# Optimization experiments

Measured on AMD Instinct MI355X. Metric: run time of the kernel, lower is better.

Reference implementation:

```python
import jax, jax.numpy as jnp
import numpy as np

SHIFT = 1  # shift_direction fixed to +1 (original picks +/-1 randomly at init)


def setup_inputs() -> dict:
    key = jax.random.key(0)
    kx, kw = jax.random.split(key)
    x = jax.random.normal(kx, (128, 128, 56, 56), dtype=jnp.float32)  # (N, C, H, W)
    w = jax.random.normal(kw, (32, 3, 128), dtype=jnp.float32)        # (out_ch, ktap, in_ch)
    return {"x": x, "w": w}


def reference(x, w):
    # roll along W (original dim 3), then 1x3 conv along W with SAME padding,
    # then roll the output along H (original dim 2).
    xr = jnp.roll(x, SHIFT, axis=3)
    # einsum 'nkmilo,jki->njmlo' == correlation: y[n,j,h,w] = sum_{k,i} xr[n,i,h,w+k-1] * w[j,k,i]
    kernel = jnp.transpose(w, (0, 2, 1))[:, :, None, :]  # (O=32, I=128, kh=1, kw=3)
    y = jax.lax.conv_general_dilated(
        xr, kernel,
        window_strides=(1, 1),
        padding=((0, 0), (1, 1)),
        dimension_numbers=("NCHW", "OIHW", "NCHW"),
    )  # (128, 32, 56, 56)
    return jnp.roll(y, SHIFT, axis=2)
```

## Files before the change

### kernel.cpp

```cpp
#include <hip/hip_runtime.h>
#include <stddef.h>


#define C_IN   128
#define C_OUT  32
#define HH     56
#define WW     56
#define HW     3136
#define KTOT   384
#define WSTRIDE 392
#define XSTRIDE 136
#define XROWSZ (57 * XSTRIDE)

typedef short bf16x8 __attribute__((ext_vector_type(8)));
typedef float f32x4  __attribute__((ext_vector_type(4)));

static __device__ __forceinline__ unsigned short f2b(float f) {
    unsigned u = __builtin_bit_cast(unsigned, f);
    unsigned r = u + 0x7FFFu + ((u >> 16) & 1u);
    return (unsigned short)(r >> 16);
}

__global__ void pack_w_kernel(const float* __restrict__ w, unsigned short* __restrict__ ws) {
    int idx = blockIdx.x * 256 + threadIdx.x;
    if (idx < C_OUT * WSTRIDE) {
        int j = idx / WSTRIDE;
        int r = idx % WSTRIDE;
        ws[idx] = f2b(r < KTOT ? w[j * KTOT + r] : 0.0f);
    }
}

__global__ __launch_bounds__(256, 2)
void conv_mfma_kernel(const float* __restrict__ x, const unsigned short* __restrict__ ws,
                      float* __restrict__ out) {
    const int bid  = blockIdx.x;
    const int n    = bid / (HH / 4);
    const int h0   = (bid % (HH / 4)) * 4;
    const int tid  = threadIdx.x;
    const int lane = tid & 63;
    const int grp  = tid >> 6;

    __shared__ __align__(16) unsigned short XT[4 * XROWSZ];

    if (tid < 68) {
        int r = tid / 17, off = (tid % 17) * 8;
        *(uint4*)&XT[r * XROWSZ + WW * XSTRIDE + off] = make_uint4(0, 0, 0, 0);
    }

    const float* xb = x + (size_t)n * (C_IN * HW);

    {
        const int q  = lane;
        const int r  = q / 14;
        const int c4 = q % 14;
        const int hs = (h0 + 55 + r) % HH;
        const size_t rowoff = (size_t)hs * WW + c4 * 4;
        unsigned short* dst0 = &XT[r * XROWSZ + (c4 * 4) * XSTRIDE];
#pragma unroll 8
        for (int p = 0; p < 32; ++p) {
            const int ch = p * 4 + grp;
            if (q < WW) {
                const float4 v = *(const float4*)(xb + (size_t)ch * HW + rowoff);
                unsigned short* dst = dst0 + ch;
                dst[0]           = f2b(v.x);
                dst[XSTRIDE]     = f2b(v.y);
                dst[2 * XSTRIDE] = f2b(v.z);
                dst[3 * XSTRIDE] = f2b(v.w);
            }
        }
    }
    __syncthreads();

    const int l15 = lane & 15;
    const int kb  = (lane >> 4) * 8;
    const unsigned short* Xr = &XT[grp * XROWSZ];

    const unsigned short* bp[4][3];
#pragma unroll
    for (int ct = 0; ct < 4; ++ct) {
        const int nn = ct * 16 + l15;
        const int cc0 = (nn >= 1 && nn <= 55) ? (nn + 54) % WW : WW;
        const int cc1 = (nn <= 55) ? (nn + 55) % WW : WW;
        const int cc2 = (nn <= 54) ? nn : WW;
        bp[ct][0] = Xr + cc0 * XSTRIDE + kb;
        bp[ct][1] = Xr + cc1 * XSTRIDE + kb;
        bp[ct][2] = Xr + cc2 * XSTRIDE + kb;
    }

    const unsigned short* wp = ws + l15 * WSTRIDE + kb;

    f32x4 acc[4][2];
#pragma unroll
    for (int ct = 0; ct < 4; ++ct) {
        acc[ct][0] = (f32x4){0.f, 0.f, 0.f, 0.f};
        acc[ct][1] = (f32x4){0.f, 0.f, 0.f, 0.f};
    }

#pragma unroll
    for (int c = 0; c < 12; ++c) {
        const int tap = c >> 2;
        const int ib  = (c & 3) * 32;
        bf16x8 A0 = *(const bf16x8*)(wp + c * 32);
        bf16x8 A1 = *(const bf16x8*)(wp + 16 * WSTRIDE + c * 32);
#pragma unroll
        for (int ct = 0; ct < 4; ++ct) {
            bf16x8 B = *(const bf16x8*)(bp[ct][tap] + ib);
            acc[ct][0] = __builtin_amdgcn_mfma_f32_16x16x32_bf16(A0, B, acc[ct][0], 0, 0, 0);
            acc[ct][1] = __builtin_amdgcn_mfma_f32_16x16x32_bf16(A1, B, acc[ct][1], 0, 0, 0);
        }
    }

    {
        const int h  = h0 + grp;
        const int j0 = (lane >> 4) * 4;
        float* ob = out + (size_t)n * (C_OUT * HW) + (size_t)h * WW;
#pragma unroll
        for (int ct = 0; ct < 4; ++ct) {
            const int nn = ct * 16 + l15;
            if (nn < WW) {
#pragma unroll
                for (int r = 0; r < 4; ++r) {
                    ob[(size_t)(j0 + r) * HW + nn]      = acc[ct][0][r];
                    ob[(size_t)(j0 + r + 16) * HW + nn] = acc[ct][1][r];
                }
            }
        }
    }
}

extern "C" void kernel_launch(void* const* d_in, const int* in_sizes, int n_in,
                              void* d_out, int out_size, void* d_ws, size_t ws_size,
                              hipStream_t stream) {
    const float* x = (const float*)d_in[0];
    const float* w = (const float*)d_in[1];
    float* out = (float*)d_out;
    unsigned short* ws = (unsigned short*)d_ws;

    pack_w_kernel<<<(C_OUT * WSTRIDE + 255) / 256, 256, 0, stream>>>(w, ws);
    conv_mfma_kernel<<<dim3(128 * (HH / 4)), dim3(256), 0, stream>>>(x, ws, out);
}
```

Measured before the change: 304.5 us.

## Double block size to 512 threads, splitting each row's columns across two waves

Raises the conv kernel's block size from 256 to 512 threads (8 waves). The staging loop now has 8 waves each loading 16 channels, and in the compute phase two waves share each output row, each handling half of the column tiles. The aim is more waves in flight to hide global-load latency during staging, with fewer accumulators per thread. In exchange each wave reuses its A-fragment weight loads across fewer MFMAs, and the launch bounds now request 4 blocks of 512 threads per CU, which may be limited by LDS.

```diff
diff --git a/kernel.cpp b/kernel.cpp
--- a/kernel.cpp
+++ b/kernel.cpp
@@ -30,7 +30,7 @@
     }
 }
 
-__global__ __launch_bounds__(256, 2)
+__global__ __launch_bounds__(512, 4)
 void conv_mfma_kernel(const float* __restrict__ x, const unsigned short* __restrict__ ws,
                       float* __restrict__ out) {
     const int bid  = blockIdx.x;
@@ -55,13 +55,13 @@
         const int c4 = q % 14;
         const int hs = (h0 + 55 + r) % HH;
         const size_t rowoff = (size_t)hs * WW + c4 * 4;
-        unsigned short* dst0 = &XT[r * XROWSZ + (c4 * 4) * XSTRIDE];
+        unsigned short* dst0 = &XT[r * XROWSZ + (c4 * 4) * XSTRIDE + grp];
+        const float* src0 = xb + (size_t)grp * HW + rowoff;
 #pragma unroll 8
-        for (int p = 0; p < 32; ++p) {
-            const int ch = p * 4 + grp;
+        for (int p = 0; p < 16; ++p) {
             if (q < WW) {
-                const float4 v = *(const float4*)(xb + (size_t)ch * HW + rowoff);
-                unsigned short* dst = dst0 + ch;
+                const float4 v = *(const float4*)(src0 + (size_t)(p * 8) * HW);
+                unsigned short* dst = dst0 + p * 8;
                 dst[0]           = f2b(v.x);
                 dst[XSTRIDE]     = f2b(v.y);
                 dst[2 * XSTRIDE] = f2b(v.z);
@@ -73,27 +73,29 @@
 
     const int l15 = lane & 15;
     const int kb  = (lane >> 4) * 8;
-    const unsigned short* Xr = &XT[grp * XROWSZ];
+    const int rr  = grp >> 1;
+    const int hf  = grp & 1;
+    const unsigned short* Xr = &XT[rr * XROWSZ];
 
-    const unsigned short* bp[4][3];
+    const unsigned short* bp[2][3];
 #pragma unroll
-    for (int ct = 0; ct < 4; ++ct) {
-        const int nn = ct * 16 + l15;
+    for (int ct2 = 0; ct2 < 2; ++ct2) {
+        const int nn = (hf * 2 + ct2) * 16 + l15;
         const int cc0 = (nn >= 1 && nn <= 55) ? (nn + 54) % WW : WW;
         const int cc1 = (nn <= 55) ? (nn + 55) % WW : WW;
         const int cc2 = (nn <= 54) ? nn : WW;
-        bp[ct][0] = Xr + cc0 * XSTRIDE + kb;
-        bp[ct][1] = Xr + cc1 * XSTRIDE + kb;
-        bp[ct][2] = Xr + cc2 * XSTRIDE + kb;
+        bp[ct2][0] = Xr + cc0 * XSTRIDE + kb;
+        bp[ct2][1] = Xr + cc1 * XSTRIDE + kb;
+        bp[ct2][2] = Xr + cc2 * XSTRIDE + kb;
     }
 
     const unsigned short* wp = ws + l15 * WSTRIDE + kb;
 
-    f32x4 acc[4][2];
+    f32x4 acc[2][2];
 #pragma unroll
-    for (int ct = 0; ct < 4; ++ct) {
-        acc[ct][0] = (f32x4){0.f, 0.f, 0.f, 0.f};
-        acc[ct][1] = (f32x4){0.f, 0.f, 0.f, 0.f};
+    for (int ct2 = 0; ct2 < 2; ++ct2) {
+        acc[ct2][0] = (f32x4){0.f, 0.f, 0.f, 0.f};
+        acc[ct2][1] = (f32x4){0.f, 0.f, 0.f, 0.f};
     }
 
 #pragma unroll
@@ -103,25 +105,25 @@
         bf16x8 A0 = *(const bf16x8*)(wp + c * 32);
         bf16x8 A1 = *(const bf16x8*)(wp + 16 * WSTRIDE + c * 32);
 #pragma unroll
-        for (int ct = 0; ct < 4; ++ct) {
-            bf16x8 B = *(const bf16x8*)(bp[ct][tap] + ib);
-            acc[ct][0] = __builtin_amdgcn_mfma_f32_16x16x32_bf16(A0, B, acc[ct][0], 0, 0, 0);
-            acc[ct][1] = __builtin_amdgcn_mfma_f32_16x16x32_bf16(A1, B, acc[ct][1], 0, 0, 0);
+        for (int ct2 = 0; ct2 < 2; ++ct2) {
+            bf16x8 B = *(const bf16x8*)(bp[ct2][tap] + ib);
+            acc[ct2][0] = __builtin_amdgcn_mfma_f32_16x16x32_bf16(A0, B, acc[ct2][0], 0, 0, 0);
+            acc[ct2][1] = __builtin_amdgcn_mfma_f32_16x16x32_bf16(A1, B, acc[ct2][1], 0, 0, 0);
         }
     }
 
     {
-        const int h  = h0 + grp;
+        const int h  = h0 + rr;
         const int j0 = (lane >> 4) * 4;
         float* ob = out + (size_t)n * (C_OUT * HW) + (size_t)h * WW;
 #pragma unroll
-        for (int ct = 0; ct < 4; ++ct) {
-            const int nn = ct * 16 + l15;
+        for (int ct2 = 0; ct2 < 2; ++ct2) {
+            const int nn = (hf * 2 + ct2) * 16 + l15;
             if (nn < WW) {
 #pragma unroll
                 for (int r = 0; r < 4; ++r) {
-                    ob[(size_t)(j0 + r) * HW + nn]      = acc[ct][0][r];
-                    ob[(size_t)(j0 + r + 16) * HW + nn] = acc[ct][1][r];
+                    ob[(size_t)(j0 + r) * HW + nn]      = acc[ct2][0][r];
+                    ob[(size_t)(j0 + r + 16) * HW + nn] = acc[ct2][1][r];
                 }
             }
         }
@@ -137,5 +139,5 @@
     unsigned short* ws = (unsigned short*)d_ws;
 
     pack_w_kernel<<<(C_OUT * WSTRIDE + 255) / 256, 256, 0, stream>>>(w, ws);
-    conv_mfma_kernel<<<dim3(128 * (HH / 4)), dim3(256), 0, stream>>>(x, ws, out);
+    conv_mfma_kernel<<<dim3(128 * (HH / 4)), dim3(512), 0, stream>>>(x, ws, out);
 }
```

Measured after the change: 307.9 us. No clear change (+1.1%).

## Use single-wave workgroups per row with packed bf16 LDS stores and XCD swizzle

Applied to the files above, without the earlier changes.

Restructures the conv kernel from 4-wave blocks covering four output rows to one-wave blocks handling a single row, which removes the block barrier in favour of an lgkmcnt wait. The staging loop now loads 8 channels per lane and converts pairs with v_cvt_pk_bf16_f32, writing 128-bit LDS stores instead of scalar 16-bit stores. Block indices are remapped so consecutive workgroups spread across the 8 XCDs. The change targets the cost of staging and conversion plus synchronization, at the price of smaller blocks and more workgroups to schedule.

```diff
diff --git a/kernel.cpp b/kernel.cpp
--- a/kernel.cpp
+++ b/kernel.cpp
@@ -21,6 +21,12 @@
     return (unsigned short)(r >> 16);
 }
 
+static __device__ __forceinline__ unsigned pk2(float lo, float hi) {
+    unsigned r;
+    asm("v_cvt_pk_bf16_f32 %0, %1, %2" : "=v"(r) : "v"(lo), "v"(hi));
+    return r;
+}
+
 __global__ void pack_w_kernel(const float* __restrict__ w, unsigned short* __restrict__ ws) {
     int idx = blockIdx.x * 256 + threadIdx.x;
     if (idx < C_OUT * WSTRIDE) {
@@ -30,50 +36,49 @@
     }
 }
 
-__global__ __launch_bounds__(256, 2)
+__global__ __launch_bounds__(64, 4)
 void conv_mfma_kernel(const float* __restrict__ x, const unsigned short* __restrict__ ws,
                       float* __restrict__ out) {
-    const int bid  = blockIdx.x;
-    const int n    = bid / (HH / 4);
-    const int h0   = (bid % (HH / 4)) * 4;
-    const int tid  = threadIdx.x;
-    const int lane = tid & 63;
-    const int grp  = tid >> 6;
+    const int bid = blockIdx.x;
+    const int wg  = (bid & 7) * 896 + (bid >> 3);
+    const int n   = wg / HH;
+    const int h   = wg % HH;
+    const int hs  = (h + HH - 1) % HH;
+    const int lane = threadIdx.x;
 
-    __shared__ __align__(16) unsigned short XT[4 * XROWSZ];
+    __shared__ __align__(16) unsigned short XT[XROWSZ];
 
-    if (tid < 68) {
-        int r = tid / 17, off = (tid % 17) * 8;
-        *(uint4*)&XT[r * XROWSZ + WW * XSTRIDE + off] = make_uint4(0, 0, 0, 0);
-    }
-
-    const float* xb = x + (size_t)n * (C_IN * HW);
+    if (lane < 17) *(uint4*)&XT[WW * XSTRIDE + lane * 8] = make_uint4(0, 0, 0, 0);
 
     {
-        const int q  = lane;
-        const int r  = q / 14;
-        const int c4 = q % 14;
-        const int hs = (h0 + 55 + r) % HH;
-        const size_t rowoff = (size_t)hs * WW + c4 * 4;
-        unsigned short* dst0 = &XT[r * XROWSZ + (c4 * 4) * XSTRIDE];
-#pragma unroll 8
-        for (int p = 0; p < 32; ++p) {
-            const int ch = p * 4 + grp;
-            if (q < WW) {
-                const float4 v = *(const float4*)(xb + (size_t)ch * HW + rowoff);
-                unsigned short* dst = dst0 + ch;
-                dst[0]           = f2b(v.x);
-                dst[XSTRIDE]     = f2b(v.y);
-                dst[2 * XSTRIDE] = f2b(v.z);
-                dst[3 * XSTRIDE] = f2b(v.w);
+        const int c4    = lane % 14;
+        const int chsub = lane / 14;
+        const float* sbase = x + (size_t)n * (C_IN * HW) + (size_t)hs * WW + c4 * 4
+                               + (size_t)(chsub * 8) * HW;
+        if (lane < WW) {
+#pragma unroll
+            for (int p = 0; p < 4; ++p) {
+                f32x4 v[8];
+#pragma unroll
+                for (int k = 0; k < 8; ++k)
+                    v[k] = *(const f32x4*)(sbase + (size_t)(p * 32 + k) * HW);
+                const int chb = p * 32 + chsub * 8;
+#pragma unroll
+                for (int vc = 0; vc < 4; ++vc) {
+                    uint4 w128;
+                    w128.x = pk2(v[0][vc], v[1][vc]);
+                    w128.y = pk2(v[2][vc], v[3][vc]);
+                    w128.z = pk2(v[4][vc], v[5][vc]);
+                    w128.w = pk2(v[6][vc], v[7][vc]);
+                    *(uint4*)&XT[(c4 * 4 + vc) * XSTRIDE + chb] = w128;
+                }
             }
         }
     }
-    __syncthreads();
+    asm volatile("s_waitcnt lgkmcnt(0)" ::: "memory");
 
     const int l15 = lane & 15;
     const int kb  = (lane >> 4) * 8;
-    const unsigned short* Xr = &XT[grp * XROWSZ];
 
     const unsigned short* bp[4][3];
 #pragma unroll
@@ -82,9 +87,9 @@
         const int cc0 = (nn >= 1 && nn <= 55) ? (nn + 54) % WW : WW;
         const int cc1 = (nn <= 55) ? (nn + 55) % WW : WW;
         const int cc2 = (nn <= 54) ? nn : WW;
-        bp[ct][0] = Xr + cc0 * XSTRIDE + kb;
-        bp[ct][1] = Xr + cc1 * XSTRIDE + kb;
-        bp[ct][2] = Xr + cc2 * XSTRIDE + kb;
+        bp[ct][0] = XT + cc0 * XSTRIDE + kb;
+        bp[ct][1] = XT + cc1 * XSTRIDE + kb;
+        bp[ct][2] = XT + cc2 * XSTRIDE + kb;
     }
 
     const unsigned short* wp = ws + l15 * WSTRIDE + kb;
@@ -111,7 +116,6 @@
     }
 
     {
-        const int h  = h0 + grp;
         const int j0 = (lane >> 4) * 4;
         float* ob = out + (size_t)n * (C_OUT * HW) + (size_t)h * WW;
 #pragma unroll
@@ -137,5 +141,5 @@
     unsigned short* ws = (unsigned short*)d_ws;
 
     pack_w_kernel<<<(C_OUT * WSTRIDE + 255) / 256, 256, 0, stream>>>(w, ws);
-    conv_mfma_kernel<<<dim3(128 * (HH / 4)), dim3(256), 0, stream>>>(x, ws, out);
+    conv_mfma_kernel<<<dim3(128 * HH), dim3(64), 0, stream>>>(x, ws, out);
 }
```

Measured after the change: 311.7 us. 1.02x slower.
